# Performance work log

Measured on AMD Instinct MI355X. Metric: run time of the kernel, lower is better.

The kernel has to match this reference:

```python
import jax, jax.numpy as jnp
import numpy as np

N, E, L, D_IN = 20000, 320000, 3, 128
K, H = 8, 64
NEG_SLOPE = 0.01


def setup_inputs() -> dict:
    key = jax.random.key(0)
    k1, k2, k3, k4, k5, k6 = jax.random.split(key, 6)
    return {
        "node_feat": jax.random.normal(k1, (N, D_IN), jnp.float32),
        "edge_feat": jax.random.normal(k2, (E, L, D_IN), jnp.float32),
        "W_enc": jax.random.normal(k3, (D_IN, K * H), jnp.float32) * (1.0 / np.sqrt(D_IN)),
        "attn_l": jax.random.normal(k4, (1, K, H), jnp.float32) * 0.1,
        "W_r": jax.random.normal(k5, (K, D_IN), jnp.float32) * (1.0 / np.sqrt(D_IN)),
        "dst": jax.random.randint(k6, (E,), 0, N, jnp.int32),
    }


def reference(node_feat, edge_feat, W_enc, attn_l, W_r, dst):
    n = node_feat.shape[0]
    e_cnt = edge_feat.shape[0]
    # metapath instance encoder ('linear'): mean over metapath length, then project
    ft = jnp.mean(edge_feat, axis=1) @ W_enc            # (E, K*H)
    ft = ft.reshape(e_cnt, K, H)                        # (E, K, H)
    # per-edge / per-dst attention logits
    el = jnp.sum(ft * attn_l, axis=-1)                  # (E, K)
    er = node_feat @ W_r.T                              # (N, K)
    e = jax.nn.leaky_relu(el + er[dst], negative_slope=NEG_SLOPE)  # (E, K)
    # edge_softmax: segmented (per destination node) stable softmax
    seg_max = jax.ops.segment_max(e, dst, num_segments=n)
    seg_max = jnp.where(jnp.isfinite(seg_max), seg_max, 0.0)
    ex = jnp.exp(e - seg_max[dst])                      # (E, K)
    seg_sum = jax.ops.segment_sum(ex, dst, num_segments=n)
    a = ex / seg_sum[dst]                               # (E, K)  (attn_drop=0 in eval)
    # weighted scatter-sum of edge features into destination nodes
    out = jax.ops.segment_sum(ft * a[..., None], dst, num_segments=n)  # (N, K, H)
    return out
```

## Files before the change

### kernel.cpp

```cpp
#include <hip/hip_runtime.h>
#include <math.h>

#define NN   20000
#define EE   320000
#define DIN  128
#define KK   8
#define HH   64
#define NEG  0.01f

__device__ __forceinline__ float wave_sum(float v) {
#pragma unroll
  for (int m = 1; m < 64; m <<= 1) v += __shfl_xor(v, m, 64);
  return v;
}

__global__ __launch_bounds__(256) void k_v(const float* __restrict__ W_enc,
                                           const float* __restrict__ attn_l,
                                           float* __restrict__ V) {
  int gid = blockIdx.x * 256 + threadIdx.x;
  if (gid < DIN * KK) {
    int d = gid >> 3, k = gid & 7;
    float acc = 0.f;
#pragma unroll 8
    for (int h = 0; h < HH; ++h)
      acc += W_enc[(long)d * 512 + k * 64 + h] * attn_l[k * 64 + h];
    V[d * 8 + k] = acc;
  }
}

__global__ __launch_bounds__(256) void k_er(const float* __restrict__ node_feat,
                                            const float* __restrict__ W_r,
                                            float* __restrict__ er) {
  __shared__ __align__(16) float4 wr4[KK * 32];
  int tid = threadIdx.x;
  if (tid < 256) wr4[tid] = ((const float4*)W_r)[tid];
  __syncthreads();
  int gid = blockIdx.x * 256 + tid;
  int n = gid >> 3, k = gid & 7;
  if (n < NN) {
    const float4* nf4 = (const float4*)node_feat + (long)n * 32;
    float acc = 0.f;
#pragma unroll
    for (int i = 0; i < 32; ++i) {
      float4 a = nf4[i], b = wr4[k * 32 + i];
      acc += a.x * b.x + a.y * b.y + a.z * b.z + a.w * b.w;
    }
    er[gid] = acc;
  }
}

__global__ __launch_bounds__(256) void k_mean_logits(
    const float* __restrict__ edge_feat, const float* __restrict__ V,
    const float* __restrict__ er, const int* __restrict__ dst,
    float* __restrict__ x, float* __restrict__ e_log) {
  int lane = threadIdx.x & 63;
  int gw = (blockIdx.x * 256 + (int)threadIdx.x) >> 6;
  const float4* V4 = (const float4*)V;
  float4 va0 = V4[lane * 4 + 0];
  float4 va1 = V4[lane * 4 + 1];
  float4 vb0 = V4[lane * 4 + 2];
  float4 vb1 = V4[lane * 4 + 3];
  const float2* ef2 = (const float2*)edge_feat;
#pragma unroll 1
  for (int t = 0; t < 4; ++t) {
    int e = gw * 4 + t;
    if (e >= EE) break;
    long b = (long)e * 192;
    float2 r0 = ef2[b + lane];
    float2 r1 = ef2[b + 64 + lane];
    float2 r2 = ef2[b + 128 + lane];
    float x0 = (r0.x + r1.x + r2.x) * (1.f / 3.f);
    float x1 = (r0.y + r1.y + r2.y) * (1.f / 3.f);
    ((float2*)x)[(long)e * 64 + lane] = make_float2(x0, x1);
    float p0 = x0 * va0.x + x1 * vb0.x;
    float p1 = x0 * va0.y + x1 * vb0.y;
    float p2 = x0 * va0.z + x1 * vb0.z;
    float p3 = x0 * va0.w + x1 * vb0.w;
    float p4 = x0 * va1.x + x1 * vb1.x;
    float p5 = x0 * va1.y + x1 * vb1.y;
    float p6 = x0 * va1.z + x1 * vb1.z;
    float p7 = x0 * va1.w + x1 * vb1.w;
    p0 = wave_sum(p0); p1 = wave_sum(p1); p2 = wave_sum(p2); p3 = wave_sum(p3);
    p4 = wave_sum(p4); p5 = wave_sum(p5); p6 = wave_sum(p6); p7 = wave_sum(p7);
    if (lane == 0) {
      int dv = dst[e];
      float4 ea = ((const float4*)er)[dv * 2 + 0];
      float4 eb = ((const float4*)er)[dv * 2 + 1];
      float z0 = p0 + ea.x, z1 = p1 + ea.y, z2 = p2 + ea.z, z3 = p3 + ea.w;
      float z4 = p4 + eb.x, z5 = p5 + eb.y, z6 = p6 + eb.z, z7 = p7 + eb.w;
      float4 o0 = make_float4(z0 > 0.f ? z0 : NEG * z0, z1 > 0.f ? z1 : NEG * z1,
                              z2 > 0.f ? z2 : NEG * z2, z3 > 0.f ? z3 : NEG * z3);
      float4 o1 = make_float4(z4 > 0.f ? z4 : NEG * z4, z5 > 0.f ? z5 : NEG * z5,
                              z6 > 0.f ? z6 : NEG * z6, z7 > 0.f ? z7 : NEG * z7);
      ((float4*)e_log)[(long)e * 2 + 0] = o0;
      ((float4*)e_log)[(long)e * 2 + 1] = o1;
    }
  }
}

__global__ __launch_bounds__(256) void k_hist(const int* __restrict__ dst,
                                              int* __restrict__ counts) {
  int e = blockIdx.x * 256 + threadIdx.x;
  if (e < EE) atomicAdd(&counts[dst[e]], 1);
}

__global__ __launch_bounds__(1024) void k_scan(const int* __restrict__ counts,
                                               int* __restrict__ offs,
                                               int* __restrict__ cursor) {
  __shared__ int wsum[16], wpre[16];
  __shared__ int running;
  int tid = threadIdx.x, lane = tid & 63, wid = tid >> 6;
  if (tid == 0) running = 0;
  __syncthreads();
  for (int base = 0; base < NN; base += 1024) {
    int i = base + tid;
    int v = (i < NN) ? counts[i] : 0;
    int incl = v;
#pragma unroll
    for (int off = 1; off < 64; off <<= 1) {
      int t = __shfl_up(incl, off, 64);
      if (lane >= off) incl += t;
    }
    if (lane == 63) wsum[wid] = incl;
    __syncthreads();
    if (tid < 16) {
      int sv = wsum[tid];
#pragma unroll
      for (int off = 1; off < 16; off <<= 1) {
        int t = __shfl_up(sv, off, 64);
        if (tid >= off) sv += t;
      }
      wpre[tid] = sv;
    }
    __syncthreads();
    int wexcl = (wid == 0) ? 0 : wpre[wid - 1];
    int excl = running + wexcl + (incl - v);
    if (i < NN) { offs[i] = excl; cursor[i] = excl; }
    int tot = wpre[15];
    __syncthreads();
    if (tid == 0) running += tot;
    __syncthreads();
  }
  if (threadIdx.x == 0) offs[NN] = running;
}

__global__ __launch_bounds__(256) void k_fill(const int* __restrict__ dst,
                                              int* __restrict__ cursor,
                                              int* __restrict__ elist) {
  int e = blockIdx.x * 256 + threadIdx.x;
  if (e < EE) {
    int p = atomicAdd(&cursor[dst[e]], 1);
    elist[p] = e;
  }
}

__global__ __launch_bounds__(256) void k_agg(const int* __restrict__ offs,
                                             const int* __restrict__ elist,
                                             const float* __restrict__ e_log,
                                             const float* __restrict__ x,
                                             float* __restrict__ y) {
  __shared__ float maxs[8], invs[8];
  __shared__ float red[4][8];
  __shared__ __align__(16) float4 xs4[32 * 32];
  __shared__ __align__(16) float wbuf[32 * 8];
  int n = blockIdx.x;
  int tid = threadIdx.x, lane = tid & 63, wid = tid >> 6;
  int start = offs[n], end = offs[n + 1];

  float m[8];
#pragma unroll
  for (int k = 0; k < 8; ++k) m[k] = -3.4e38f;
  for (int i = start + tid; i < end; i += 256) {
    long e = elist[i];
    float4 a = ((const float4*)e_log)[e * 2 + 0];
    float4 b = ((const float4*)e_log)[e * 2 + 1];
    m[0] = fmaxf(m[0], a.x); m[1] = fmaxf(m[1], a.y);
    m[2] = fmaxf(m[2], a.z); m[3] = fmaxf(m[3], a.w);
    m[4] = fmaxf(m[4], b.x); m[5] = fmaxf(m[5], b.y);
    m[6] = fmaxf(m[6], b.z); m[7] = fmaxf(m[7], b.w);
  }
#pragma unroll
  for (int k = 0; k < 8; ++k) {
#pragma unroll
    for (int mm = 1; mm < 64; mm <<= 1) m[k] = fmaxf(m[k], __shfl_xor(m[k], mm, 64));
  }
  if (lane == 0) {
#pragma unroll
    for (int k = 0; k < 8; ++k) red[wid][k] = m[k];
  }
  __syncthreads();
  if (tid < 8)
    maxs[tid] = fmaxf(fmaxf(red[0][tid], red[1][tid]), fmaxf(red[2][tid], red[3][tid]));
  __syncthreads();
  float mk[8];
#pragma unroll
  for (int k = 0; k < 8; ++k) mk[k] = maxs[k];

  float s[8];
#pragma unroll
  for (int k = 0; k < 8; ++k) s[k] = 0.f;
  for (int i = start + tid; i < end; i += 256) {
    long e = elist[i];
    float4 a = ((const float4*)e_log)[e * 2 + 0];
    float4 b = ((const float4*)e_log)[e * 2 + 1];
    s[0] += __expf(a.x - mk[0]); s[1] += __expf(a.y - mk[1]);
    s[2] += __expf(a.z - mk[2]); s[3] += __expf(a.w - mk[3]);
    s[4] += __expf(b.x - mk[4]); s[5] += __expf(b.y - mk[5]);
    s[6] += __expf(b.z - mk[6]); s[7] += __expf(b.w - mk[7]);
  }
#pragma unroll
  for (int k = 0; k < 8; ++k) s[k] = wave_sum(s[k]);
  if (lane == 0) {
#pragma unroll
    for (int k = 0; k < 8; ++k) red[wid][k] = s[k];
  }
  __syncthreads();
  if (tid < 8) {
    float tot = red[0][tid] + red[1][tid] + red[2][tid] + red[3][tid];
    invs[tid] = tot > 0.f ? 1.f / tot : 0.f;
  }
  __syncthreads();

  float acc0 = 0.f, acc1 = 0.f, acc2 = 0.f, acc3 = 0.f;
  int d = tid & 127, kg = tid >> 7;
  const float* xs = (const float*)xs4;
  for (int base = start; base < end; base += 32) {
    int nb = min(32, end - base);
    for (int j = tid; j < nb * 32; j += 256) {
      long e = elist[base + (j >> 5)];
      xs4[j] = ((const float4*)x)[e * 32 + (j & 31)];
    }
    if (tid < nb * 8) {
      long e = elist[base + (tid >> 3)];
      int k = tid & 7;
      wbuf[tid] = __expf(e_log[e * 8 + k] - maxs[k]) * invs[k];
    }
    __syncthreads();
    for (int j = 0; j < nb; ++j) {
      float xv = xs[j * 128 + d];
      float4 wv = *(const float4*)&wbuf[j * 8 + kg * 4];
      acc0 += wv.x * xv; acc1 += wv.y * xv; acc2 += wv.z * xv; acc3 += wv.w * xv;
    }
    __syncthreads();
  }
  float* yp = y + (long)n * 1024 + kg * 512 + d;
  yp[0]   = acc0;
  yp[128] = acc1;
  yp[256] = acc2;
  yp[384] = acc3;
}

__global__ __launch_bounds__(256) void k_out(const float* __restrict__ y,
                                             const float* __restrict__ W_enc,
                                             float* __restrict__ out) {
  __shared__ __align__(16) float ys[32 * 128];
  __shared__ __align__(16) float ws[128 * 64];
  int k = blockIdx.y, n0 = blockIdx.x * 32;
  int tid = threadIdx.x;
  for (int i = tid; i < 32 * 128; i += 256) {
    int r = i >> 7, dd = i & 127;
    ys[i] = y[(long)(n0 + r) * 1024 + k * 128 + dd];
  }
  for (int i = tid; i < 128 * 64; i += 256) {
    int h = i & 63, dd = i >> 6;
    ws[dd * 64 + h] = W_enc[(long)dd * 512 + k * 64 + h];
  }
  __syncthreads();
  int h = tid & 63, rg = tid >> 6;
  float acc[8] = {0.f, 0.f, 0.f, 0.f, 0.f, 0.f, 0.f, 0.f};
  for (int d4 = 0; d4 < 32; ++d4) {
    float w0 = ws[(d4 * 4 + 0) * 64 + h];
    float w1 = ws[(d4 * 4 + 1) * 64 + h];
    float w2 = ws[(d4 * 4 + 2) * 64 + h];
    float w3 = ws[(d4 * 4 + 3) * 64 + h];
#pragma unroll
    for (int i = 0; i < 8; ++i) {
      float4 yv = *(const float4*)&ys[(rg * 8 + i) * 128 + d4 * 4];
      acc[i] += yv.x * w0 + yv.y * w1 + yv.z * w2 + yv.w * w3;
    }
  }
#pragma unroll
  for (int i = 0; i < 8; ++i)
    out[(long)(n0 + rg * 8 + i) * 512 + k * 64 + h] = acc[i];
}

extern "C" void kernel_launch(void* const* d_in, const int* in_sizes, int n_in,
                              void* d_out, int out_size, void* d_ws, size_t ws_size,
                              hipStream_t stream) {
  const float* node_feat = (const float*)d_in[0];
  const float* edge_feat = (const float*)d_in[1];
  const float* W_enc     = (const float*)d_in[2];
  const float* attn_l    = (const float*)d_in[3];
  const float* W_r       = (const float*)d_in[4];
  const int*   dst       = (const int*)d_in[5];
  float* out = (float*)d_out;

  char* ws = (char*)d_ws;
  size_t off = 0;
  auto carve = [&](size_t bytes) {
    void* p = ws + off;
    off = (off + bytes + 255) & ~(size_t)255;
    return p;
  };
  float* x      = (float*)carve((size_t)EE * DIN * 4);
  float* er     = (float*)carve((size_t)NN * KK * 4);
  float* V      = (float*)carve((size_t)DIN * KK * 4);
  float* e_log  = (float*)carve((size_t)EE * KK * 4);
  int*   counts = (int*)carve((size_t)NN * 4);
  int*   offs   = (int*)carve((size_t)(NN + 1) * 4);
  int*   cursor = (int*)carve((size_t)NN * 4);
  int*   elist  = (int*)carve((size_t)EE * 4);
  float* y      = (float*)carve((size_t)NN * KK * DIN * 4);
  (void)ws_size; (void)in_sizes; (void)n_in; (void)out_size;

  hipMemsetAsync(counts, 0, (size_t)NN * 4, stream);

  k_v  <<<4, 256, 0, stream>>>(W_enc, attn_l, V);
  k_er <<<(NN * KK) / 256, 256, 0, stream>>>(node_feat, W_r, er);
  k_mean_logits<<<EE / 16, 256, 0, stream>>>(edge_feat, V, er, dst, x, e_log);
  k_hist<<<EE / 256, 256, 0, stream>>>(dst, counts);
  k_scan<<<1, 1024, 0, stream>>>(counts, offs, cursor);
  k_fill<<<EE / 256, 256, 0, stream>>>(dst, cursor, elist);
  k_agg <<<NN, 256, 0, stream>>>(offs, elist, e_log, x, y);
  k_out <<<dim3(NN / 32, KK), 256, 0, stream>>>(y, W_enc, out);
}
```

Before: 954.4 us.

## Store intermediates in bf16 and use MFMA for logits and output projection

Edge means and aggregated node features are now stored as bf16, halving the traffic for the large intermediate x and y buffers. Logit computation and the final W_enc projection use 16x16x32 bf16 MFMA instructions in place of wave reductions and scalar FMA loops. The histogram is folded into the logit kernel, and the single-block scan becomes a three-kernel multi-block scan. Rounding to bf16 adds error to the attention inputs and the output.

```diff
diff --git a/kernel.cpp b/kernel.cpp
--- a/kernel.cpp
+++ b/kernel.cpp
@@ -8,24 +8,47 @@
 #define HH   64
 #define NEG  0.01f
 
+typedef __attribute__((ext_vector_type(8))) short short8;
+typedef __attribute__((ext_vector_type(4))) float f32x4;
+
+__device__ __forceinline__ unsigned short f2bf(float f) {
+  unsigned u = __float_as_uint(f);
+  u += 0x7FFF + ((u >> 16) & 1);
+  return (unsigned short)(u >> 16);
+}
+__device__ __forceinline__ float bf2f_lo(unsigned u) {
+  return __uint_as_float(u << 16);
+}
+__device__ __forceinline__ float bf2f_hi(unsigned u) {
+  return __uint_as_float(u & 0xFFFF0000u);
+}
+
 __device__ __forceinline__ float wave_sum(float v) {
 #pragma unroll
   for (int m = 1; m < 64; m <<= 1) v += __shfl_xor(v, m, 64);
   return v;
 }
 
-__global__ __launch_bounds__(256) void k_v(const float* __restrict__ W_enc,
-                                           const float* __restrict__ attn_l,
-                                           float* __restrict__ V) {
+__global__ __launch_bounds__(256) void k_vt(const float* __restrict__ W_enc,
+                                            const float* __restrict__ attn_l,
+                                            unsigned short* __restrict__ Vt) {
   int gid = blockIdx.x * 256 + threadIdx.x;
-  if (gid < DIN * KK) {
-    int d = gid >> 3, k = gid & 7;
-    float acc = 0.f;
+  if (gid >= 16 * 128) return;
+  int n = gid >> 7, d = gid & 127;
+  float acc = 0.f;
+  if (n < 8) {
 #pragma unroll 8
     for (int h = 0; h < HH; ++h)
-      acc += W_enc[(long)d * 512 + k * 64 + h] * attn_l[k * 64 + h];
-    V[d * 8 + k] = acc;
-  }
+      acc += W_enc[(size_t)d * 512 + n * 64 + h] * attn_l[n * 64 + h];
+  }
+  Vt[gid] = f2bf(acc);
+}
+
+__global__ __launch_bounds__(256) void k_wt(const float* __restrict__ W_enc,
+                                            unsigned short* __restrict__ Wt) {
+  int gid = blockIdx.x * 256 + threadIdx.x;
+  int row = gid >> 7, d = gid & 127;
+  Wt[gid] = f2bf(W_enc[(size_t)d * 512 + row]);
 }
 
 __global__ __launch_bounds__(256) void k_er(const float* __restrict__ node_feat,
@@ -38,7 +61,7 @@
   int gid = blockIdx.x * 256 + tid;
   int n = gid >> 3, k = gid & 7;
   if (n < NN) {
-    const float4* nf4 = (const float4*)node_feat + (long)n * 32;
+    const float4* nf4 = (const float4*)node_feat + (size_t)n * 32;
     float acc = 0.f;
 #pragma unroll
     for (int i = 0; i < 32; ++i) {
@@ -49,99 +72,112 @@
   }
 }
 
-__global__ __launch_bounds__(256) void k_mean_logits(
-    const float* __restrict__ edge_feat, const float* __restrict__ V,
-    const float* __restrict__ er, const int* __restrict__ dst,
-    float* __restrict__ x, float* __restrict__ e_log) {
+__global__ __launch_bounds__(256) void k_mean(const float* __restrict__ ef,
+                                              unsigned short* __restrict__ x) {
+  size_t gid = (size_t)blockIdx.x * 256 + threadIdx.x;
+  size_t e = gid >> 4;
+  int s = gid & 15;
+  const float4* p = (const float4*)(ef + e * 384) + s * 2;
+  float4 a0 = p[0],  a1 = p[1];
+  float4 b0 = p[32], b1 = p[33];
+  float4 c0 = p[64], c1 = p[65];
+  const float i3 = 1.f / 3.f;
+  float m0 = (a0.x + b0.x + c0.x) * i3, m1 = (a0.y + b0.y + c0.y) * i3;
+  float m2 = (a0.z + b0.z + c0.z) * i3, m3 = (a0.w + b0.w + c0.w) * i3;
+  float m4 = (a1.x + b1.x + c1.x) * i3, m5 = (a1.y + b1.y + c1.y) * i3;
+  float m6 = (a1.z + b1.z + c1.z) * i3, m7 = (a1.w + b1.w + c1.w) * i3;
+  uint4 o;
+  o.x = (unsigned)f2bf(m0) | ((unsigned)f2bf(m1) << 16);
+  o.y = (unsigned)f2bf(m2) | ((unsigned)f2bf(m3) << 16);
+  o.z = (unsigned)f2bf(m4) | ((unsigned)f2bf(m5) << 16);
+  o.w = (unsigned)f2bf(m6) | ((unsigned)f2bf(m7) << 16);
+  ((uint4*)x)[gid] = o;
+}
+
+__global__ __launch_bounds__(256) void k_logit(const unsigned short* __restrict__ x,
+                                               const unsigned short* __restrict__ Vt,
+                                               const float* __restrict__ er,
+                                               const int* __restrict__ dst,
+                                               float* __restrict__ e_log,
+                                               int* __restrict__ counts) {
   int lane = threadIdx.x & 63;
   int gw = (blockIdx.x * 256 + (int)threadIdx.x) >> 6;
-  const float4* V4 = (const float4*)V;
-  float4 va0 = V4[lane * 4 + 0];
-  float4 va1 = V4[lane * 4 + 1];
-  float4 vb0 = V4[lane * 4 + 2];
-  float4 vb1 = V4[lane * 4 + 3];
-  const float2* ef2 = (const float2*)edge_feat;
-#pragma unroll 1
-  for (int t = 0; t < 4; ++t) {
-    int e = gw * 4 + t;
-    if (e >= EE) break;
-    long b = (long)e * 192;
-    float2 r0 = ef2[b + lane];
-    float2 r1 = ef2[b + 64 + lane];
-    float2 r2 = ef2[b + 128 + lane];
-    float x0 = (r0.x + r1.x + r2.x) * (1.f / 3.f);
-    float x1 = (r0.y + r1.y + r2.y) * (1.f / 3.f);
-    ((float2*)x)[(long)e * 64 + lane] = make_float2(x0, x1);
-    float p0 = x0 * va0.x + x1 * vb0.x;
-    float p1 = x0 * va0.y + x1 * vb0.y;
-    float p2 = x0 * va0.z + x1 * vb0.z;
-    float p3 = x0 * va0.w + x1 * vb0.w;
-    float p4 = x0 * va1.x + x1 * vb1.x;
-    float p5 = x0 * va1.y + x1 * vb1.y;
-    float p6 = x0 * va1.z + x1 * vb1.z;
-    float p7 = x0 * va1.w + x1 * vb1.w;
-    p0 = wave_sum(p0); p1 = wave_sum(p1); p2 = wave_sum(p2); p3 = wave_sum(p3);
-    p4 = wave_sum(p4); p5 = wave_sum(p5); p6 = wave_sum(p6); p7 = wave_sum(p7);
-    if (lane == 0) {
+  int e0 = gw * 16;
+  int m = lane & 15, quad = lane >> 4;
+  const short8* xr = (const short8*)(x + (size_t)(e0 + m) * 128);
+  const short8* vr = (const short8*)(Vt + (size_t)m * 128);
+  f32x4 acc = {0.f, 0.f, 0.f, 0.f};
+#pragma unroll
+  for (int kt = 0; kt < 4; ++kt) {
+    short8 a = xr[kt * 4 + quad];
+    short8 b = vr[kt * 4 + quad];
+    acc = __builtin_amdgcn_mfma_f32_16x16x32_bf16(a, b, acc, 0, 0, 0);
+  }
+  if (m < 8) {
+#pragma unroll
+    for (int r = 0; r < 4; ++r) {
+      int e = e0 + quad * 4 + r;
       int dv = dst[e];
-      float4 ea = ((const float4*)er)[dv * 2 + 0];
-      float4 eb = ((const float4*)er)[dv * 2 + 1];
-      float z0 = p0 + ea.x, z1 = p1 + ea.y, z2 = p2 + ea.z, z3 = p3 + ea.w;
-      float z4 = p4 + eb.x, z5 = p5 + eb.y, z6 = p6 + eb.z, z7 = p7 + eb.w;
-      float4 o0 = make_float4(z0 > 0.f ? z0 : NEG * z0, z1 > 0.f ? z1 : NEG * z1,
-                              z2 > 0.f ? z2 : NEG * z2, z3 > 0.f ? z3 : NEG * z3);
-      float4 o1 = make_float4(z4 > 0.f ? z4 : NEG * z4, z5 > 0.f ? z5 : NEG * z5,
-                              z6 > 0.f ? z6 : NEG * z6, z7 > 0.f ? z7 : NEG * z7);
-      ((float4*)e_log)[(long)e * 2 + 0] = o0;
-      ((float4*)e_log)[(long)e * 2 + 1] = o1;
-    }
-  }
-}
-
-__global__ __launch_bounds__(256) void k_hist(const int* __restrict__ dst,
-                                              int* __restrict__ counts) {
-  int e = blockIdx.x * 256 + threadIdx.x;
-  if (e < EE) atomicAdd(&counts[dst[e]], 1);
-}
-
-__global__ __launch_bounds__(1024) void k_scan(const int* __restrict__ counts,
+      float z = acc[r] + er[dv * 8 + m];
+      z = z > 0.f ? z : NEG * z;
+      e_log[(size_t)e * 8 + m] = z;
+      if (m == 0) atomicAdd(&counts[dv], 1);
+    }
+  }
+}
+
+__device__ __forceinline__ int block_excl_scan256(int v, int tid) {
+  __shared__ int wtot[4];
+  int lane = tid & 63, wid = tid >> 6;
+  int incl = v;
+#pragma unroll
+  for (int off = 1; off < 64; off <<= 1) {
+    int t = __shfl_up(incl, off, 64);
+    if (lane >= off) incl += t;
+  }
+  if (lane == 63) wtot[wid] = incl;
+  __syncthreads();
+  if (tid == 0) {
+    int s = 0;
+#pragma unroll
+    for (int i = 0; i < 4; ++i) { int t = wtot[i]; wtot[i] = s; s += t; }
+  }
+  __syncthreads();
+  return wtot[wid] + incl - v;
+}
+
+__global__ __launch_bounds__(256) void k_scan1(const int* __restrict__ counts,
+                                               int* __restrict__ lexcl,
+                                               int* __restrict__ btot) {
+  int b = blockIdx.x, tid = threadIdx.x;
+  int i = b * 256 + tid;
+  int v = (i < NN) ? counts[i] : 0;
+  int ex = block_excl_scan256(v, tid);
+  lexcl[i] = ex;
+  if (tid == 255) btot[b] = ex + v;
+}
+
+__global__ __launch_bounds__(256) void k_scan2(int* __restrict__ btot,
+                                               int* __restrict__ bbase,
+                                               int* __restrict__ offs) {
+  int tid = threadIdx.x;
+  int v = (tid < 80) ? btot[tid] : 0;
+  int ex = block_excl_scan256(v, tid);
+  if (tid < 80) bbase[tid] = ex;
+  if (tid == 0) offs[NN] = EE;
+}
+
+__global__ __launch_bounds__(256) void k_scan3(const int* __restrict__ lexcl,
+                                               const int* __restrict__ bbase,
                                                int* __restrict__ offs,
                                                int* __restrict__ cursor) {
-  __shared__ int wsum[16], wpre[16];
-  __shared__ int running;
-  int tid = threadIdx.x, lane = tid & 63, wid = tid >> 6;
-  if (tid == 0) running = 0;
-  __syncthreads();
-  for (int base = 0; base < NN; base += 1024) {
-    int i = base + tid;
-    int v = (i < NN) ? counts[i] : 0;
-    int incl = v;
-#pragma unroll
-    for (int off = 1; off < 64; off <<= 1) {
-      int t = __shfl_up(incl, off, 64);
-      if (lane >= off) incl += t;
-    }
-    if (lane == 63) wsum[wid] = incl;
-    __syncthreads();
-    if (tid < 16) {
-      int sv = wsum[tid];
-#pragma unroll
-      for (int off = 1; off < 16; off <<= 1) {
-        int t = __shfl_up(sv, off, 64);
-        if (tid >= off) sv += t;
-      }
-      wpre[tid] = sv;
-    }
-    __syncthreads();
-    int wexcl = (wid == 0) ? 0 : wpre[wid - 1];
-    int excl = running + wexcl + (incl - v);
-    if (i < NN) { offs[i] = excl; cursor[i] = excl; }
-    int tot = wpre[15];
-    __syncthreads();
-    if (tid == 0) running += tot;
-    __syncthreads();
-  }
-  if (threadIdx.x == 0) offs[NN] = running;
+  int b = blockIdx.x, tid = threadIdx.x;
+  int i = b * 256 + tid;
+  if (i < NN) {
+    int o = lexcl[i] + bbase[b];
+    offs[i] = o;
+    cursor[i] = o;
+  }
 }
 
 __global__ __launch_bounds__(256) void k_fill(const int* __restrict__ dst,
@@ -157,11 +193,11 @@
 __global__ __launch_bounds__(256) void k_agg(const int* __restrict__ offs,
                                              const int* __restrict__ elist,
                                              const float* __restrict__ e_log,
-                                             const float* __restrict__ x,
-                                             float* __restrict__ y) {
+                                             const unsigned short* __restrict__ x,
+                                             unsigned short* __restrict__ y) {
   __shared__ float maxs[8], invs[8];
   __shared__ float red[4][8];
-  __shared__ __align__(16) float4 xs4[32 * 32];
+  __shared__ __align__(16) float xs[32 * 128];
   __shared__ __align__(16) float wbuf[32 * 8];
   int n = blockIdx.x;
   int tid = threadIdx.x, lane = tid & 63, wid = tid >> 6;
@@ -171,7 +207,7 @@
 #pragma unroll
   for (int k = 0; k < 8; ++k) m[k] = -3.4e38f;
   for (int i = start + tid; i < end; i += 256) {
-    long e = elist[i];
+    size_t e = (size_t)elist[i];
     float4 a = ((const float4*)e_log)[e * 2 + 0];
     float4 b = ((const float4*)e_log)[e * 2 + 1];
     m[0] = fmaxf(m[0], a.x); m[1] = fmaxf(m[1], a.y);
@@ -200,7 +236,7 @@
 #pragma unroll
   for (int k = 0; k < 8; ++k) s[k] = 0.f;
   for (int i = start + tid; i < end; i += 256) {
-    long e = elist[i];
+    size_t e = (size_t)elist[i];
     float4 a = ((const float4*)e_log)[e * 2 + 0];
     float4 b = ((const float4*)e_log)[e * 2 + 1];
     s[0] += __expf(a.x - mk[0]); s[1] += __expf(a.y - mk[1]);
@@ -223,15 +259,18 @@
 
   float acc0 = 0.f, acc1 = 0.f, acc2 = 0.f, acc3 = 0.f;
   int d = tid & 127, kg = tid >> 7;
-  const float* xs = (const float*)xs4;
   for (int base = start; base < end; base += 32) {
     int nb = min(32, end - base);
-    for (int j = tid; j < nb * 32; j += 256) {
-      long e = elist[base + (j >> 5)];
-      xs4[j] = ((const float4*)x)[e * 32 + (j & 31)];
+    for (int j = tid; j < nb * 16; j += 256) {
+      size_t e = (size_t)elist[base + (j >> 4)];
+      uint4 t = ((const uint4*)x)[e * 16 + (j & 15)];
+      float4 lo = make_float4(bf2f_lo(t.x), bf2f_hi(t.x), bf2f_lo(t.y), bf2f_hi(t.y));
+      float4 hi = make_float4(bf2f_lo(t.z), bf2f_hi(t.z), bf2f_lo(t.w), bf2f_hi(t.w));
+      ((float4*)xs)[(j >> 4) * 32 + (j & 15) * 2 + 0] = lo;
+      ((float4*)xs)[(j >> 4) * 32 + (j & 15) * 2 + 1] = hi;
     }
     if (tid < nb * 8) {
-      long e = elist[base + (tid >> 3)];
+      size_t e = (size_t)elist[base + (tid >> 3)];
       int k = tid & 7;
       wbuf[tid] = __expf(e_log[e * 8 + k] - maxs[k]) * invs[k];
     }
@@ -243,45 +282,34 @@
     }
     __syncthreads();
   }
-  float* yp = y + (long)n * 1024 + kg * 512 + d;
-  yp[0]   = acc0;
-  yp[128] = acc1;
-  yp[256] = acc2;
-  yp[384] = acc3;
-}
-
-__global__ __launch_bounds__(256) void k_out(const float* __restrict__ y,
-                                             const float* __restrict__ W_enc,
+  size_t yb = ((size_t)n * 8 + kg * 4) * 128 + d;
+  y[yb + 0 * 128] = f2bf(acc0);
+  y[yb + 1 * 128] = f2bf(acc1);
+  y[yb + 2 * 128] = f2bf(acc2);
+  y[yb + 3 * 128] = f2bf(acc3);
+}
+
+__global__ __launch_bounds__(256) void k_out(const unsigned short* __restrict__ y,
+                                             const unsigned short* __restrict__ Wt,
                                              float* __restrict__ out) {
-  __shared__ __align__(16) float ys[32 * 128];
-  __shared__ __align__(16) float ws[128 * 64];
-  int k = blockIdx.y, n0 = blockIdx.x * 32;
-  int tid = threadIdx.x;
-  for (int i = tid; i < 32 * 128; i += 256) {
-    int r = i >> 7, dd = i & 127;
-    ys[i] = y[(long)(n0 + r) * 1024 + k * 128 + dd];
-  }
-  for (int i = tid; i < 128 * 64; i += 256) {
-    int h = i & 63, dd = i >> 6;
-    ws[dd * 64 + h] = W_enc[(long)dd * 512 + k * 64 + h];
-  }
-  __syncthreads();
-  int h = tid & 63, rg = tid >> 6;
-  float acc[8] = {0.f, 0.f, 0.f, 0.f, 0.f, 0.f, 0.f, 0.f};
-  for (int d4 = 0; d4 < 32; ++d4) {
-    float w0 = ws[(d4 * 4 + 0) * 64 + h];
-    float w1 = ws[(d4 * 4 + 1) * 64 + h];
-    float w2 = ws[(d4 * 4 + 2) * 64 + h];
-    float w3 = ws[(d4 * 4 + 3) * 64 + h];
-#pragma unroll
-    for (int i = 0; i < 8; ++i) {
-      float4 yv = *(const float4*)&ys[(rg * 8 + i) * 128 + d4 * 4];
-      acc[i] += yv.x * w0 + yv.y * w1 + yv.z * w2 + yv.w * w3;
-    }
-  }
-#pragma unroll
-  for (int i = 0; i < 8; ++i)
-    out[(long)(n0 + rg * 8 + i) * 512 + k * 64 + h] = acc[i];
+  int kh = blockIdx.y;
+  int n0 = blockIdx.x * 16;
+  int wv = threadIdx.x >> 6;
+  int lane = threadIdx.x & 63;
+  int m = lane & 15, quad = lane >> 4;
+  int h0 = wv * 16;
+  const short8* ar = (const short8*)(y + ((size_t)(n0 + m) * 8 + kh) * 128);
+  const short8* br = (const short8*)(Wt + (size_t)(kh * 64 + h0 + m) * 128);
+  f32x4 acc = {0.f, 0.f, 0.f, 0.f};
+#pragma unroll
+  for (int kt = 0; kt < 4; ++kt) {
+    short8 a = ar[kt * 4 + quad];
+    short8 b = br[kt * 4 + quad];
+    acc = __builtin_amdgcn_mfma_f32_16x16x32_bf16(a, b, acc, 0, 0, 0);
+  }
+#pragma unroll
+  for (int r = 0; r < 4; ++r)
+    out[(size_t)(n0 + quad * 4 + r) * 512 + kh * 64 + h0 + m] = acc[r];
 }
 
 extern "C" void kernel_launch(void* const* d_in, const int* in_sizes, int n_in,
@@ -302,25 +330,32 @@
     off = (off + bytes + 255) & ~(size_t)255;
     return p;
   };
-  float* x      = (float*)carve((size_t)EE * DIN * 4);
-  float* er     = (float*)carve((size_t)NN * KK * 4);
-  float* V      = (float*)carve((size_t)DIN * KK * 4);
-  float* e_log  = (float*)carve((size_t)EE * KK * 4);
-  int*   counts = (int*)carve((size_t)NN * 4);
-  int*   offs   = (int*)carve((size_t)(NN + 1) * 4);
-  int*   cursor = (int*)carve((size_t)NN * 4);
-  int*   elist  = (int*)carve((size_t)EE * 4);
-  float* y      = (float*)carve((size_t)NN * KK * DIN * 4);
+  unsigned short* x   = (unsigned short*)carve((size_t)EE * DIN * 2);
+  unsigned short* y   = (unsigned short*)carve((size_t)NN * KK * DIN * 2);
+  unsigned short* Vt  = (unsigned short*)carve(16 * 128 * 2);
+  unsigned short* Wt  = (unsigned short*)carve((size_t)KK * HH * DIN * 2);
+  float* er    = (float*)carve((size_t)NN * KK * 4);
+  float* e_log = (float*)carve((size_t)EE * KK * 4);
+  int* counts  = (int*)carve((size_t)20480 * 4);
+  int* lexcl   = (int*)carve((size_t)20480 * 4);
+  int* btot    = (int*)carve(80 * 4);
+  int* bbase   = (int*)carve(80 * 4);
+  int* offs    = (int*)carve((size_t)(NN + 1) * 4);
+  int* cursor  = (int*)carve((size_t)NN * 4);
+  int* elist   = (int*)carve((size_t)EE * 4);
   (void)ws_size; (void)in_sizes; (void)n_in; (void)out_size;
 
   hipMemsetAsync(counts, 0, (size_t)NN * 4, stream);
 
-  k_v  <<<4, 256, 0, stream>>>(W_enc, attn_l, V);
-  k_er <<<(NN * KK) / 256, 256, 0, stream>>>(node_feat, W_r, er);
-  k_mean_logits<<<EE / 16, 256, 0, stream>>>(edge_feat, V, er, dst, x, e_log);
-  k_hist<<<EE / 256, 256, 0, stream>>>(dst, counts);
-  k_scan<<<1, 1024, 0, stream>>>(counts, offs, cursor);
+  k_vt  <<<8, 256, 0, stream>>>(W_enc, attn_l, Vt);
+  k_wt  <<<256, 256, 0, stream>>>(W_enc, Wt);
+  k_er  <<<(NN * KK) / 256, 256, 0, stream>>>(node_feat, W_r, er);
+  k_mean<<<(EE * 16) / 256, 256, 0, stream>>>(edge_feat, x);
+  k_logit<<<EE / 64, 256, 0, stream>>>(x, Vt, er, dst, e_log, counts);
+  k_scan1<<<80, 256, 0, stream>>>(counts, lexcl, btot);
+  k_scan2<<<1, 256, 0, stream>>>(btot, bbase, offs);
+  k_scan3<<<80, 256, 0, stream>>>(lexcl, bbase, offs, cursor);
   k_fill<<<EE / 256, 256, 0, stream>>>(dst, cursor, elist);
   k_agg <<<NN, 256, 0, stream>>>(offs, elist, e_log, x, y);
-  k_out <<<dim3(NN / 32, KK), 256, 0, stream>>>(y, W_enc, out);
-}
+  k_out <<<dim3(NN / 16, KK), 256, 0, stream>>>(y, Wt, out);
+}
```

Result: faster. 867.3 us (-9.1%).
